# Kernel tuning notes

Hardware: AMD Instinct MI355X
Metric: run time of the kernel (lower is better)

The kernel has to match this reference:

```python
import jax, jax.numpy as jnp
import numpy as np

EMBED = 768
HEADS = 12
HEAD_DIM = EMBED // HEADS
DEPTH = 4
PATCH = 16
GRID = 32  # 512 / 16
MLP_DIM = 4 * EMBED
LN_EPS = 1e-5


def layer_norm(x, w, b):
    m = jnp.mean(x, axis=-1, keepdims=True)
    v = jnp.mean(jnp.square(x - m), axis=-1, keepdims=True)
    return (x - m) * jax.lax.rsqrt(v + LN_EPS) * w + b


def sam_attention(x, qkv_w, qkv_b, proj_w, proj_b, rel_pos_h, rel_pos_w):
    B, H, W, C = x.shape
    N = H * W
    scale = HEAD_DIM ** -0.5
    qkv = x.reshape(B, N, C) @ qkv_w + qkv_b  # (B, N, 3C)
    qkv = qkv.reshape(B, N, 3, HEADS, HEAD_DIM).transpose(2, 0, 3, 1, 4)
    qkv = qkv.reshape(3, B * HEADS, N, HEAD_DIM)
    q, k, v = qkv[0], qkv[1], qkv[2]
    attn = jnp.einsum('bqc,bkc->bqk', q * scale, k)  # (B*nh, N, N)
    # decomposed relative position (q_size == k_size, table already max_rel_dist)
    idx_h = jnp.arange(H)[:, None] - jnp.arange(H)[None, :] + (H - 1)
    idx_w = jnp.arange(W)[:, None] - jnp.arange(W)[None, :] + (W - 1)
    Rh = rel_pos_h[idx_h]  # (H, H, hd)
    Rw = rel_pos_w[idx_w]  # (W, W, hd)
    r_q = q.reshape(B * HEADS, H, W, HEAD_DIM)
    rel_h = jnp.einsum('bhwc,hkc->bhwk', r_q, Rh)
    rel_w = jnp.einsum('bhwc,wkc->bhwk', r_q, Rw)
    attn = (attn.reshape(B * HEADS, H, W, H, W)
            + rel_h[:, :, :, :, None]
            + rel_w[:, :, :, None, :]).reshape(B * HEADS, N, N)
    attn = jax.nn.softmax(attn, axis=-1)
    out = (attn @ v).reshape(B, HEADS, H, W, HEAD_DIM)
    out = out.transpose(0, 2, 3, 1, 4).reshape(B, H, W, C)
    return out @ proj_w + proj_b


def setup_inputs() -> dict:
    key = jax.random.key(0)
    ks = jax.random.split(key, 20)
    s = lambda k, shape, sc=0.02: jax.random.normal(k, shape, jnp.float32) * sc
    inp = {
        'x': jax.random.normal(ks[0], (4, 3, 512, 512), jnp.float32),
        'conv_w': s(ks[1], (EMBED, 3, PATCH, PATCH)),
        'conv_b': jnp.zeros((EMBED,), jnp.float32),
        'pos_embed': s(ks[2], (1, GRID, GRID, EMBED)),
        'ln1_w': jnp.ones((DEPTH, EMBED), jnp.float32),
        'ln1_b': jnp.zeros((DEPTH, EMBED), jnp.float32),
        'qkv_w': s(ks[3], (DEPTH, EMBED, 3 * EMBED)),
        'qkv_b': jnp.zeros((DEPTH, 3 * EMBED), jnp.float32),
        'proj_w': s(ks[4], (DEPTH, EMBED, EMBED)),
        'proj_b': jnp.zeros((DEPTH, EMBED), jnp.float32),
        'rel_pos_h': s(ks[5], (DEPTH, 2 * GRID - 1, HEAD_DIM)),
        'rel_pos_w': s(ks[6], (DEPTH, 2 * GRID - 1, HEAD_DIM)),
        'ln2_w': jnp.ones((DEPTH, EMBED), jnp.float32),
        'ln2_b': jnp.zeros((DEPTH, EMBED), jnp.float32),
        'fc1_w': s(ks[7], (DEPTH, EMBED, MLP_DIM)),
        'fc1_b': jnp.zeros((DEPTH, MLP_DIM), jnp.float32),
        'fc2_w': s(ks[8], (DEPTH, MLP_DIM, EMBED)),
        'fc2_b': jnp.zeros((DEPTH, EMBED), jnp.float32),
    }
    return inp


def reference(x, conv_w, conv_b, pos_embed, ln1_w, ln1_b, qkv_w, qkv_b,
              proj_w, proj_b, rel_pos_h, rel_pos_w, ln2_w, ln2_b,
              fc1_w, fc1_b, fc2_w, fc2_b):
    # patch embed: conv stride=patch, then NCHW -> NHWC
    h = jax.lax.conv_general_dilated(
        x, conv_w, window_strides=(PATCH, PATCH), padding='VALID',
        dimension_numbers=('NCHW', 'OIHW', 'NCHW'))
    h = h.transpose(0, 2, 3, 1) + conv_b  # (B, 32, 32, 768)
    h = h + pos_embed
    for i in range(DEPTH):
        a = sam_attention(layer_norm(h, ln1_w[i], ln1_b[i]),
                          qkv_w[i], qkv_b[i], proj_w[i], proj_b[i],
                          rel_pos_h[i], rel_pos_w[i])
        h = h + a
        m = layer_norm(h, ln2_w[i], ln2_b[i])
        m = jax.nn.gelu(m @ fc1_w[i] + fc1_b[i], approximate=False) @ fc2_w[i] + fc2_b[i]
        h = h + m
    return h
```

## Files before the change

kernel.cpp:

```cpp
#include <hip/hip_runtime.h>
#include <hip/hip_bf16.h>
#include <math.h>
#include <stdint.h>

#define EMBED 768
#define NTOK  1024
#define BATCH 4
#define NHEAD 12
#define HD    64
#define MLPD  3072
#define M_ROWS 4096

typedef __attribute__((ext_vector_type(8))) short short8;
typedef __attribute__((ext_vector_type(4))) float floatx4;

__device__ __forceinline__ float b2f(__hip_bfloat16 v) { return __bfloat162float(v); }

__device__ __forceinline__ void gld_lds16(const void* g, void* l) {
    __builtin_amdgcn_global_load_lds(
        (const __attribute__((address_space(1))) uint32_t*)g,
        (__attribute__((address_space(3))) uint32_t*)l, 16, 0, 0);
}

__device__ __forceinline__ int swz(int row, int c) { return row*64 + (((c) ^ (row & 7)) << 3); }

__device__ __forceinline__ void xcd_remap(int gx, int gy, int& bx, int& by) {
    int id  = blockIdx.x + gx*blockIdx.y;
    int nwg = gx*gy;
    int q = nwg >> 3, r = nwg & 7;
    int xcd = id & 7, idx = id >> 3;
    int nid = (xcd < r ? xcd*(q+1) : r*(q+1) + (xcd-r)*q) + idx;
    bx = nid % gx;
    by = nid / gx;
}

__global__ __launch_bounds__(256)
void im2col(const float* __restrict__ x, __hip_bfloat16* __restrict__ A)
{
    int p  = blockIdx.x;
    int b  = p >> 10;
    int n  = p & 1023;
    int gh = n >> 5, gw = n & 31;
    int tid = threadIdx.x;
    for (int i = tid; i < 768; i += 256) {
        int ci = i >> 8, r = i & 255, kh = r >> 4, kw = r & 15;
        A[(size_t)p*768 + i] = __float2bfloat16(
            x[(((size_t)b*3 + ci)*512 + (gh*16 + kh))*512 + gw*16 + kw]);
    }
}

__global__ __launch_bounds__(256)
void cvt_bf16(const float* __restrict__ in, __hip_bfloat16* __restrict__ out, int n)
{
    int i = blockIdx.x*256 + threadIdx.x;
    if (i < n) out[i] = __float2bfloat16(in[i]);
}

__global__ __launch_bounds__(256)
void layernorm_bf16(const float* __restrict__ in,
                    const float* __restrict__ w,
                    const float* __restrict__ b,
                    __hip_bfloat16* __restrict__ out)
{
    int row = blockIdx.x;
    const float* xr = in + (size_t)row*768;
    int tid = threadIdx.x;
    float v0 = xr[tid], v1 = xr[tid+256], v2 = xr[tid+512];
    float s = v0+v1+v2, ss = v0*v0+v1*v1+v2*v2;
    __shared__ float rs[256], rss[256];
    rs[tid] = s; rss[tid] = ss; __syncthreads();
    for (int o = 128; o > 0; o >>= 1) {
        if (tid < o) { rs[tid] += rs[tid+o]; rss[tid] += rss[tid+o]; }
        __syncthreads();
    }
    float mean = rs[0] * (1.f/768.f);
    float var  = rss[0] * (1.f/768.f) - mean*mean;
    float inv  = rsqrtf(var + 1e-5f);
    out[(size_t)row*768 + tid]     = __float2bfloat16((v0-mean)*inv*w[tid]     + b[tid]);
    out[(size_t)row*768 + tid+256] = __float2bfloat16((v1-mean)*inv*w[tid+256] + b[tid+256]);
    out[(size_t)row*768 + tid+512] = __float2bfloat16((v2-mean)*inv*w[tid+512] + b[tid+512]);
}

__global__ __launch_bounds__(256)
void resum_ln(float* __restrict__ h,
              const float* __restrict__ p0, const float* __restrict__ p1,
              const float* __restrict__ bias,
              const float* __restrict__ w, const float* __restrict__ b,
              __hip_bfloat16* __restrict__ out)
{
    int row = blockIdx.x;
    int tid = threadIdx.x;
    size_t base = (size_t)row*768;
    float v[3];
    float s = 0.f, ss = 0.f;
    #pragma unroll
    for (int e = 0; e < 3; ++e) {
        int i = tid + e*256;
        float val = h[base+i] + p0[base+i] + p1[base+i] + bias[i];
        h[base+i] = val;
        v[e] = val; s += val; ss += val*val;
    }
    __shared__ float rs[256], rss[256];
    rs[tid] = s; rss[tid] = ss; __syncthreads();
    for (int o = 128; o > 0; o >>= 1) {
        if (tid < o) { rs[tid] += rs[tid+o]; rss[tid] += rss[tid+o]; }
        __syncthreads();
    }
    float mean = rs[0] * (1.f/768.f);
    float var  = rss[0] * (1.f/768.f) - mean*mean;
    float inv  = rsqrtf(var + 1e-5f);
    #pragma unroll
    for (int e = 0; e < 3; ++e) {
        int i = tid + e*256;
        out[base+i] = __float2bfloat16((v[e]-mean)*inv*w[i] + b[i]);
    }
}

__global__ __launch_bounds__(256)
void resum_out(const float* __restrict__ h,
               const float* __restrict__ p0, const float* __restrict__ p1,
               const float* __restrict__ bias,
               float* __restrict__ out)
{
    int i = blockIdx.x*256 + threadIdx.x;
    out[i] = h[i] + p0[i] + p1[i] + bias[i % 768];
}

__global__ __launch_bounds__(256)
void prep_weights(const float* __restrict__ qkv_w,  const float* __restrict__ proj_w,
                  const float* __restrict__ fc1_w,  const float* __restrict__ fc2_w,
                  __hip_bfloat16* __restrict__ qkv_wt, __hip_bfloat16* __restrict__ proj_wt,
                  __hip_bfloat16* __restrict__ fc1_wt, __hip_bfloat16* __restrict__ fc2_wt)
{
    int id = blockIdx.x;
    const float* src; __hip_bfloat16* dst; int K, N, bx, by;
    if (id < 1728)      {            src = qkv_w;  dst = qkv_wt;  K = 768;  N = 2304; bx = id % 72; by = id / 72; }
    else if (id < 2304) { id -= 1728; src = proj_w; dst = proj_wt; K = 768;  N = 768;  bx = id % 24; by = id / 24; }
    else if (id < 4608) { id -= 2304; src = fc1_w;  dst = fc1_wt;  K = 768;  N = 3072; bx = id % 96; by = id / 96; }
    else                { id -= 4608; src = fc2_w;  dst = fc2_wt;  K = 3072; N = 768;  bx = id % 24; by = id / 24; }

    __shared__ float t[32][33];
    int n0 = bx*32, k0 = by*32;
    int tx = threadIdx.x & 31, ty = threadIdx.x >> 5;
    #pragma unroll
    for (int r = 0; r < 4; ++r) {
        int row = ty + r*8;
        t[row][tx] = src[(size_t)(k0+row)*N + n0 + tx];
    }
    __syncthreads();
    #pragma unroll
    for (int r = 0; r < 4; ++r) {
        int row = ty + r*8;
        dst[(size_t)(n0+row)*K + k0 + tx] = __float2bfloat16(t[tx][row]);
    }
}

__global__ __launch_bounds__(256)
void gemm64(const __hip_bfloat16* __restrict__ A,
            const __hip_bfloat16* __restrict__ Bt,
            const float* __restrict__ bias,
            const float* __restrict__ res,
            const float* __restrict__ posadd,
            float* __restrict__ Cf,
            int M, int N, int K)
{
    __shared__ __align__(16) char smem[24576];

    const int tid  = threadIdx.x;
    const int lane = tid & 63;
    const int wid  = tid >> 6;
    const int wr   = wid >> 1;
    const int wc   = wid & 1;
    const int lr   = lane & 15;
    const int quad = lane >> 4;

    int bx, by;
    xcd_remap(gridDim.x, gridDim.y, bx, by);
    const int bm = by * 64;
    const int bn = bx * 128;

    const int srow  = tid >> 2;
    const int skoff = ((tid & 3) ^ ((tid >> 3) & 3)) * 8;
    const int csw   = (quad ^ ((lr >> 1) & 3)) * 8;

    floatx4 acc[2][4];
    #pragma unroll
    for (int i = 0; i < 2; ++i)
        #pragma unroll
        for (int j = 0; j < 4; ++j)
            acc[i][j] = (floatx4){0.f,0.f,0.f,0.f};

    auto stage = [&](int bq, int k0) {
        char* base = smem + bq*12288 + (wid * 1024);
        gld_lds16(A + (size_t)(bm + srow)*K + k0 + skoff, base);
        #pragma unroll
        for (int c = 0; c < 2; ++c)
            gld_lds16(Bt + (size_t)(bn + c*64 + srow)*K + k0 + skoff,
                      base + 4096 + c*4096);
    };

    const int nt = K >> 5;
    stage(0, 0);
    stage(1, 32);
    int cur = 0;
    for (int t = 0; t < nt; ++t) {
        if (t + 1 < nt) asm volatile("s_waitcnt vmcnt(3)" ::: "memory");
        else            asm volatile("s_waitcnt vmcnt(0)" ::: "memory");
        __builtin_amdgcn_s_barrier();

        const __hip_bfloat16* As = (const __hip_bfloat16*)(smem + cur*12288);
        const __hip_bfloat16* Bs = As + 2048;

        short8 a[2], b[4];
        #pragma unroll
        for (int i = 0; i < 2; ++i)
            a[i] = *(const short8*)((const void*)(As + (wr*32 + i*16 + lr)*32 + csw));
        #pragma unroll
        for (int j = 0; j < 4; ++j)
            b[j] = *(const short8*)((const void*)(Bs + (wc*64 + j*16 + lr)*32 + csw));
        asm volatile("s_waitcnt lgkmcnt(0)" ::: "memory");
        __builtin_amdgcn_sched_barrier(0);
        __builtin_amdgcn_s_barrier();

        if (t + 2 < nt) stage(cur, (t+2)*32);

        #pragma unroll
        for (int i = 0; i < 2; ++i)
            #pragma unroll
            for (int j = 0; j < 4; ++j)
                acc[i][j] = __builtin_amdgcn_mfma_f32_16x16x32_bf16(a[i], b[j], acc[i][j], 0, 0, 0);
        cur ^= 1;
    }

    #pragma unroll
    for (int j = 0; j < 4; ++j) {
        int col = bn + wc*64 + j*16 + lr;
        float bs = bias[col];
        #pragma unroll
        for (int i = 0; i < 2; ++i) {
            #pragma unroll
            for (int r = 0; r < 4; ++r) {
                int row = bm + wr*32 + i*16 + quad*4 + r;
                float val = acc[i][j][r] + bs;
                if (res)    val += res[(size_t)row*N + col];
                if (posadd) val += posadd[(size_t)(row & 1023)*N + col];
                Cf[(size_t)row*N + col] = val;
            }
        }
    }
}

__global__ __launch_bounds__(256)
void gemm128(const __hip_bfloat16* __restrict__ A,
             const __hip_bfloat16* __restrict__ Bt,
             const float* __restrict__ bias,
             float* __restrict__ Cf,
             __hip_bfloat16* __restrict__ Cb,
             __hip_bfloat16* __restrict__ qp,
             __hip_bfloat16* __restrict__ kp,
             __hip_bfloat16* __restrict__ vp,
             int M, int N, int K, int S, int dogelu, int emode)
{
    __shared__ __align__(16) char smem[32768];

    const int tid  = threadIdx.x;
    const int lane = tid & 63;
    const int wid  = tid >> 6;
    const int wr   = wid >> 1;
    const int wc   = wid & 1;
    const int lr   = lane & 15;
    const int quad = lane >> 4;

    int bx, by;
    xcd_remap(gridDim.x, gridDim.y, bx, by);
    const int bm = by * 128;
    const int bn = bx * 128;
    const int z  = blockIdx.z;
    const int Kseg = K / S;
    const int kbeg = z * Kseg;

    const int srow  = tid >> 2;
    const int skoff = ((tid & 3) ^ ((tid >> 3) & 3)) * 8;
    const int csw   = (quad ^ ((lr >> 1) & 3)) * 8;

    floatx4 acc[4][4];
    #pragma unroll
    for (int i = 0; i < 4; ++i)
        #pragma unroll
        for (int j = 0; j < 4; ++j)
            acc[i][j] = (floatx4){0.f,0.f,0.f,0.f};

    auto stage = [&](int bq, int k0) {
        char* base = smem + bq*16384 + (wid * 1024);
        #pragma unroll
        for (int c = 0; c < 2; ++c)
            gld_lds16(A + (size_t)(bm + c*64 + srow)*K + k0 + skoff,
                      base + c*4096);
        #pragma unroll
        for (int c = 0; c < 2; ++c)
            gld_lds16(Bt + (size_t)(bn + c*64 + srow)*K + k0 + skoff,
                      base + 8192 + c*4096);
    };

    const int nt = Kseg >> 5;
    stage(0, kbeg);
    stage(1, kbeg + 32);
    int cur = 0;
    for (int t = 0; t < nt; ++t) {
        if (t + 1 < nt) asm volatile("s_waitcnt vmcnt(4)" ::: "memory");
        else            asm volatile("s_waitcnt vmcnt(0)" ::: "memory");
        __builtin_amdgcn_s_barrier();

        const __hip_bfloat16* As = (const __hip_bfloat16*)(smem + cur*16384);
        const __hip_bfloat16* Bs = As + 4096;

        short8 a[4], b[4];
        #pragma unroll
        for (int i = 0; i < 4; ++i)
            a[i] = *(const short8*)((const void*)(As + (wr*64 + i*16 + lr)*32 + csw));
        #pragma unroll
        for (int j = 0; j < 4; ++j)
            b[j] = *(const short8*)((const void*)(Bs + (wc*64 + j*16 + lr)*32 + csw));
        asm volatile("s_waitcnt lgkmcnt(0)" ::: "memory");
        __builtin_amdgcn_sched_barrier(0);
        __builtin_amdgcn_s_barrier();

        if (t + 2 < nt) stage(cur, kbeg + (t+2)*32);

        #pragma unroll
        for (int i = 0; i < 4; ++i)
            #pragma unroll
            for (int j = 0; j < 4; ++j)
                acc[i][j] = __builtin_amdgcn_mfma_f32_16x16x32_bf16(a[i], b[j], acc[i][j], 0, 0, 0);
        cur ^= 1;
    }

    if (emode == 3) {
        #pragma unroll
        for (int j = 0; j < 4; ++j) {
            int col = bn + wc*64 + j*16 + lr;
            #pragma unroll
            for (int i = 0; i < 4; ++i) {
                #pragma unroll
                for (int r = 0; r < 4; ++r) {
                    int row = bm + wr*64 + i*16 + quad*4 + r;
                    Cf[(size_t)z*M*N + (size_t)row*N + col] = acc[i][j][r];
                }
            }
        }
        return;
    }

    __hip_bfloat16* epi = (__hip_bfloat16*)(smem + wid*4864);

    if (emode == 1) {
        #pragma unroll
        for (int p = 0; p < 2; ++p) {
            #pragma unroll
            for (int j = 0; j < 4; ++j) {
                float bs = bias[bn + wc*64 + j*16 + lr];
                #pragma unroll
                for (int ii = 0; ii < 2; ++ii) {
                    int i = p*2 + ii;
                    #pragma unroll
                    for (int r = 0; r < 4; ++r) {
                        float val = acc[i][j][r] + bs;
                        if (dogelu) val = 0.5f*val*(1.f + erff(val*0.70710678118f));
                        epi[(ii*16 + quad*4 + r)*72 + j*16 + lr] = __float2bfloat16(val);
                    }
                }
            }
            #pragma unroll
            for (int p2 = 0; p2 < 4; ++p2) {
                int row = p2*8 + (lane >> 3), chunk = lane & 7;
                short8 v = *(const short8*)((const void*)(epi + row*72 + chunk*8));
                *(short8*)((void*)(Cb + (size_t)(bm + wr*64 + p*32 + row)*N
                                      + bn + wc*64 + chunk*8)) = v;
            }
        }
        return;
    }

    const int head64 = (bn + wc*64) >> 6;
    const int which  = head64 / 12;
    const int head   = head64 % 12;
    const int b_     = (bm + wr*64) >> 10;
    const int bh     = b_*NHEAD + head;
    const int n0     = (bm + wr*64) & 1023;

    if (which < 2) {
        __hip_bfloat16* dst = (which == 0 ? qp : kp) + ((size_t)bh*NTOK + n0)*HD;
        #pragma unroll
        for (int p = 0; p < 2; ++p) {
            #pragma unroll
            for (int j = 0; j < 4; ++j) {
                float bs = bias[bn + wc*64 + j*16 + lr];
                #pragma unroll
                for (int ii = 0; ii < 2; ++ii) {
                    int i = p*2 + ii;
                    #pragma unroll
                    for (int r = 0; r < 4; ++r)
                        epi[(ii*16 + quad*4 + r)*72 + j*16 + lr] =
                            __float2bfloat16(acc[i][j][r] + bs);
                }
            }
            #pragma unroll
            for (int p2 = 0; p2 < 4; ++p2) {
                int row = p2*8 + (lane >> 3), chunk = lane & 7;
                short8 v = *(const short8*)((const void*)(epi + row*72 + chunk*8));
                *(short8*)((void*)(dst + (size_t)(p*32 + row)*HD + chunk*8)) = v;
            }
        }
    } else {
        __hip_bfloat16* dstv = vp + (size_t)bh*HD*NTOK + n0;
        #pragma unroll
        for (int p = 0; p < 2; ++p) {
            #pragma unroll
            for (int j = 0; j < 4; ++j) {
                float bs = bias[bn + wc*64 + j*16 + lr];
                #pragma unroll
                for (int ii = 0; ii < 2; ++ii) {
                    int i = p*2 + ii;
                    #pragma unroll
                    for (int r = 0; r < 4; ++r)
                        epi[(j*16 + lr)*36 + ii*16 + quad*4 + r] =
                            __float2bfloat16(acc[i][j][r] + bs);
                }
            }
            #pragma unroll
            for (int p2 = 0; p2 < 4; ++p2) {
                int d = p2*16 + (lane >> 2), chunk = lane & 3;
                short8 v = *(const short8*)((const void*)(epi + d*36 + chunk*8));
                *(short8*)((void*)(dstv + (size_t)d*NTOK + p*32 + chunk*8)) = v;
            }
        }
    }
}

__global__ __launch_bounds__(256)
void attention_mfma(const __hip_bfloat16* __restrict__ qp,
                    const __hip_bfloat16* __restrict__ kp,
                    const __hip_bfloat16* __restrict__ vp,
                    const float* __restrict__ rph,
                    const float* __restrict__ rpw,
                    __hip_bfloat16* __restrict__ out)
{
    const int blk  = blockIdx.x;
    const int bh   = blk >> 4;
    const int qt   = blk & 15;
    const int b    = bh / NHEAD;
    const int head = bh % NHEAD;
    const int tid  = threadIdx.x;
    const int lane = tid & 63;
    const int w    = tid >> 6;
    const int lr   = lane & 15;
    const int quad = lane >> 4;

    __shared__ __align__(16) __hip_bfloat16 Qs[64*64];
    __shared__ __align__(16) __hip_bfloat16 Ks[64*64];
    __shared__ __align__(16) __hip_bfloat16 Vs[64*64];
    __shared__ __align__(16) __hip_bfloat16 Ps[4*16*64];
    __shared__ float relhS[64*32];
    __shared__ float relwS[64*32];

    const __hip_bfloat16* qb = qp + ((size_t)bh*NTOK + qt*64)*HD;
    const __hip_bfloat16* kb = kp + (size_t)bh*NTOK*HD;
    const __hip_bfloat16* vb = vp + (size_t)bh*HD*NTOK;

    const int sr = tid >> 2;
    const int sc = (tid & 3) * 2;

    short8 kreg0, kreg1, vreg0, vreg1;
    {
        const __hip_bfloat16* kk = kb + (size_t)sr*HD + sc*8;
        kreg0 = *(const short8*)((const void*)kk);
        kreg1 = *(const short8*)((const void*)(kk + 8));
        const __hip_bfloat16* vv = vb + (size_t)sr*NTOK + sc*8;
        vreg0 = *(const short8*)((const void*)vv);
        vreg1 = *(const short8*)((const void*)(vv + 8));
    }

    {
        const __hip_bfloat16* qq = qb + (size_t)sr*HD + sc*8;
        short8 q0 = *(const short8*)((const void*)qq);
        short8 q1 = *(const short8*)((const void*)(qq + 8));
        *(short8*)((void*)(Qs + swz(sr, sc)))   = q0;
        *(short8*)((void*)(Qs + swz(sr, sc+1))) = q1;
    }

    for (int i = tid; i < 504; i += 256) {
        int r = i >> 3, c = i & 7;
        const float* ph = rph + (size_t)r*HD + c*8;
        const float* pw = rpw + (size_t)r*HD + c*8;
        union { short8 v; __hip_bfloat16 e[8]; } uh, uw;
        #pragma unroll
        for (int e = 0; e < 8; ++e) { uh.e[e] = __float2bfloat16(ph[e]); uw.e[e] = __float2bfloat16(pw[e]); }
        *(short8*)((void*)(Ks + swz(r, c))) = uh.v;
        *(short8*)((void*)(Vs + swz(r, c))) = uw.v;
    }
    if (tid < 16) {
        short8 z = (short8){0,0,0,0,0,0,0,0};
        int c = tid & 7;
        if (tid < 8) *(short8*)((void*)(Ks + swz(63, c))) = z;
        else         *(short8*)((void*)(Vs + swz(63, c))) = z;
    }
    __syncthreads();

    short8 qa0 = *(const short8*)((const void*)(Qs + swz(w*16 + lr, quad)));
    short8 qa1 = *(const short8*)((const void*)(Qs + swz(w*16 + lr, 4 + quad)));

    const int qrow = w*16 + quad*4;
    const int qh_  = qt*2 + (w >> 1);
    const int qw_  = (w & 1)*16 + quad*4;

    #pragma unroll
    for (int j = 0; j < 4; ++j) {
        int t = j*16 + lr;
        short8 th0 = *(const short8*)((const void*)(Ks + swz(j*16 + lr, quad)));
        short8 th1 = *(const short8*)((const void*)(Ks + swz(j*16 + lr, 4 + quad)));
        floatx4 ha = (floatx4){0.f,0.f,0.f,0.f};
        ha = __builtin_amdgcn_mfma_f32_16x16x32_bf16(qa0, th0, ha, 0, 0, 0);
        ha = __builtin_amdgcn_mfma_f32_16x16x32_bf16(qa1, th1, ha, 0, 0, 0);
        short8 tw0 = *(const short8*)((const void*)(Vs + swz(j*16 + lr, quad)));
        short8 tw1 = *(const short8*)((const void*)(Vs + swz(j*16 + lr, 4 + quad)));
        floatx4 wa = (floatx4){0.f,0.f,0.f,0.f};
        wa = __builtin_amdgcn_mfma_f32_16x16x32_bf16(qa0, tw0, wa, 0, 0, 0);
        wa = __builtin_amdgcn_mfma_f32_16x16x32_bf16(qa1, tw1, wa, 0, 0, 0);
        int kh = qh_ + 31 - t;
        #pragma unroll
        for (int rr = 0; rr < 4; ++rr) {
            if (kh >= 0 && kh < 32) relhS[(qrow + rr)*32 + kh] = ha[rr];
            int kw = qw_ + rr + 31 - t;
            if (kw >= 0 && kw < 32) relwS[(qrow + rr)*32 + kw] = wa[rr];
        }
    }

    float rw[4][2];
    #pragma unroll
    for (int rr = 0; rr < 4; ++rr)
        #pragma unroll
        for (int jp = 0; jp < 2; ++jp)
            rw[rr][jp] = relwS[(qrow + rr)*32 + jp*16 + lr];

    floatx4 o[4];
    #pragma unroll
    for (int ds = 0; ds < 4; ++ds) o[ds] = (floatx4){0.f,0.f,0.f,0.f};
    float lsum[4] = {0.f, 0.f, 0.f, 0.f};

    const float scale = 0.125f;

    for (int kt = 0; kt < 16; ++kt) {
        __syncthreads();
        *(short8*)((void*)(Ks + swz(sr, sc)))   = kreg0;
        *(short8*)((void*)(Ks + swz(sr, sc+1))) = kreg1;
        *(short8*)((void*)(Vs + swz(sr, sc)))   = vreg0;
        *(short8*)((void*)(Vs + swz(sr, sc+1))) = vreg1;
        __syncthreads();

        if (kt < 15) {
            const __hip_bfloat16* kk = kb + (size_t)(kt+1)*64*HD + (size_t)sr*HD + sc*8;
            kreg0 = *(const short8*)((const void*)kk);
            kreg1 = *(const short8*)((const void*)(kk + 8));
            const __hip_bfloat16* vv = vb + (size_t)sr*NTOK + (kt+1)*64 + sc*8;
            vreg0 = *(const short8*)((const void*)vv);
            vreg1 = *(const short8*)((const void*)(vv + 8));
        }

        float2 rh2[4];
        #pragma unroll
        for (int rr = 0; rr < 4; ++rr)
            rh2[rr] = *(const float2*)((const void*)(relhS + (qrow + rr)*32 + kt*2));

        floatx4 sv[4];
        #pragma unroll
        for (int j = 0; j < 4; ++j) {
            short8 kb0 = *(const short8*)((const void*)(Ks + swz(j*16 + lr, quad)));
            short8 kb1 = *(const short8*)((const void*)(Ks + swz(j*16 + lr, 4 + quad)));
            floatx4 z = (floatx4){0.f,0.f,0.f,0.f};
            z = __builtin_amdgcn_mfma_f32_16x16x32_bf16(qa0, kb0, z, 0, 0, 0);
            z = __builtin_amdgcn_mfma_f32_16x16x32_bf16(qa1, kb1, z, 0, 0, 0);
            sv[j] = z;
        }

        #pragma unroll
        for (int j = 0; j < 4; ++j) {
            int colc = j*2 + (lr >> 3);
            #pragma unroll
            for (int rr = 0; rr < 4; ++rr) {
                float s = sv[j][rr]*scale + ((j < 2) ? rh2[rr].x : rh2[rr].y) + rw[rr][j & 1];
                s = fminf(fmaxf(s, -60.f), 60.f);
                float pp = __expf(s);
                lsum[rr] += pp;
                int prow = quad*4 + rr;
                Ps[w*1024 + prow*64 + ((colc ^ (prow & 7)) << 3) + (lr & 7)] = __float2bfloat16(pp);
            }
        }

        short8 pa0 = *(const short8*)((const void*)(Ps + w*1024 + swz(lr, quad)));
        short8 pa1 = *(const short8*)((const void*)(Ps + w*1024 + swz(lr, 4 + quad)));
        #pragma unroll
        for (int ds = 0; ds < 4; ++ds) {
            short8 v0 = *(const short8*)((const void*)(Vs + swz(ds*16 + lr, quad)));
            short8 v1 = *(const short8*)((const void*)(Vs + swz(ds*16 + lr, 4 + quad)));
            o[ds] = __builtin_amdgcn_mfma_f32_16x16x32_bf16(pa0, v0, o[ds], 0, 0, 0);
            o[ds] = __builtin_amdgcn_mfma_f32_16x16x32_bf16(pa1, v1, o[ds], 0, 0, 0);
        }
    }

    #pragma unroll
    for (int off = 1; off < 16; off <<= 1)
        #pragma unroll
        for (int rr = 0; rr < 4; ++rr)
            lsum[rr] += __shfl_xor(lsum[rr], off, 16);

    #pragma unroll
    for (int rr = 0; rr < 4; ++rr) {
        float inv = 1.f / lsum[rr];
        int n = qt*64 + w*16 + quad*4 + rr;
        size_t base = ((size_t)b*NTOK + n)*EMBED + head*HD;
        #pragma unroll
        for (int ds = 0; ds < 4; ++ds)
            out[base + ds*16 + lr] = __float2bfloat16(o[ds][rr] * inv);
    }
}

extern "C" void kernel_launch(void* const* d_in, const int* in_sizes, int n_in,
                              void* d_out, int out_size, void* d_ws, size_t ws_size,
                              hipStream_t stream)
{
    const float* x      = (const float*)d_in[0];
    const float* conv_w = (const float*)d_in[1];
    const float* conv_b = (const float*)d_in[2];
    const float* pos    = (const float*)d_in[3];
    const float* ln1_w  = (const float*)d_in[4];
    const float* ln1_b  = (const float*)d_in[5];
    const float* qkv_w  = (const float*)d_in[6];
    const float* qkv_b  = (const float*)d_in[7];
    const float* proj_w = (const float*)d_in[8];
    const float* proj_b = (const float*)d_in[9];
    const float* rph    = (const float*)d_in[10];
    const float* rpw    = (const float*)d_in[11];
    const float* ln2_w  = (const float*)d_in[12];
    const float* ln2_b  = (const float*)d_in[13];
    const float* fc1_w  = (const float*)d_in[14];
    const float* fc1_b  = (const float*)d_in[15];
    const float* fc2_w  = (const float*)d_in[16];
    const float* fc2_b  = (const float*)d_in[17];

    char* p = (char*)d_ws;
    float*           h       = (float*)p;           p += (size_t)M_ROWS*EMBED*4;
    __hip_bfloat16*  q_perm  = (__hip_bfloat16*)p;
    float*           p0      = (float*)p;           p += (size_t)48*NTOK*HD*2;
    __hip_bfloat16*  k_perm  = (__hip_bfloat16*)p;  p += (size_t)48*NTOK*HD*2;
    __hip_bfloat16*  vt_perm = (__hip_bfloat16*)p;  p += (size_t)48*NTOK*HD*2;
    __hip_bfloat16*  attn_o  = (__hip_bfloat16*)p;  p += (size_t)M_ROWS*EMBED*2;
    __hip_bfloat16*  x_ln    = (__hip_bfloat16*)p;  p += (size_t)M_ROWS*EMBED*2;
    __hip_bfloat16*  mlp     = (__hip_bfloat16*)p;  p += (size_t)M_ROWS*MLPD*2;
    __hip_bfloat16*  qkv_wt  = (__hip_bfloat16*)p;  p += (size_t)2304*768*2;
    __hip_bfloat16*  proj_wt = (__hip_bfloat16*)p;  p += (size_t)768*768*2;
    __hip_bfloat16*  fc1_wt  = (__hip_bfloat16*)p;  p += (size_t)MLPD*768*2;
    __hip_bfloat16*  fc2_wt  = (__hip_bfloat16*)p;  p += (size_t)768*MLPD*2;

    __hip_bfloat16*  A_im    = mlp;
    __hip_bfloat16*  conv_wt = qkv_wt;

    im2col<<<M_ROWS, 256, 0, stream>>>(x, A_im);
    cvt_bf16<<<(768*768 + 255)/256, 256, 0, stream>>>(conv_w, conv_wt, 768*768);
    gemm64<<<dim3(768/128, M_ROWS/64, 1), 256, 0, stream>>>(
        A_im, conv_wt, conv_b, nullptr, pos, h, M_ROWS, 768, 768);

    layernorm_bf16<<<M_ROWS, 256, 0, stream>>>(h, ln1_w, ln1_b, x_ln);

    for (int L = 0; L < 4; ++L) {
        prep_weights<<<6912, 256, 0, stream>>>(
            qkv_w + (size_t)L*768*2304, proj_w + (size_t)L*768*768,
            fc1_w + (size_t)L*768*MLPD, fc2_w + (size_t)L*MLPD*768,
            qkv_wt, proj_wt, fc1_wt, fc2_wt);

        gemm128<<<dim3(2304/128, M_ROWS/128, 1), 256, 0, stream>>>(
            x_ln, qkv_wt, qkv_b + (size_t)L*3*EMBED,
            nullptr, nullptr, q_perm, k_perm, vt_perm,
            M_ROWS, 2304, 768, 1, 0, 2);

        attention_mfma<<<48*16, 256, 0, stream>>>(
            q_perm, k_perm, vt_perm,
            rph + (size_t)L*63*64, rpw + (size_t)L*63*64, attn_o);

        gemm64<<<dim3(768/128, M_ROWS/64, 1), 256, 0, stream>>>(
            attn_o, proj_wt, proj_b + (size_t)L*EMBED, h, nullptr,
            h, M_ROWS, 768, 768);

        layernorm_bf16<<<M_ROWS, 256, 0, stream>>>(h, ln2_w + L*EMBED, ln2_b + L*EMBED, x_ln);

        gemm128<<<dim3(MLPD/128, M_ROWS/128, 1), 256, 0, stream>>>(
            x_ln, fc1_wt, fc1_b + (size_t)L*MLPD,
            nullptr, mlp, nullptr, nullptr, nullptr,
            M_ROWS, MLPD, 768, 1, 1, 1);

        gemm128<<<dim3(768/128, M_ROWS/128, 2), 256, 0, stream>>>(
            mlp, fc2_wt, nullptr,
            p0, nullptr, nullptr, nullptr, nullptr,
            M_ROWS, 768, MLPD, 2, 0, 3);

        float* p1 = p0 + (size_t)M_ROWS*768;
        if (L < 3) {
            resum_ln<<<M_ROWS, 256, 0, stream>>>(
                h, p0, p1, fc2_b + (size_t)L*EMBED,
                ln1_w + (size_t)(L+1)*EMBED, ln1_b + (size_t)(L+1)*EMBED, x_ln);
        } else {
            resum_out<<<M_ROWS*EMBED/256, 256, 0, stream>>>(
                h, p0, p1, fc2_b + (size_t)L*EMBED, (float*)d_out);
        }
    }
}
```

Measured before the change: 898.0 us.

## Triple-buffer LDS and double-buffer register fragments in GEMM main loops

Both GEMM kernels go from a two-stage LDS ring to a three-stage ring, and the loop is unrolled by two with ping-pong register fragments. LDS reads for the next K-step are issued before the MFMAs of the current step, so LDS latency overlaps with matrix math, and global prefetch runs one tile further ahead. The cost is more shared memory per block (36KB and 48KB), which may lower occupancy, plus extra registers for the second fragment set. The loop assumes an even number of K tiles per segment.

Result: slower. 920.8 us (+2.5%).

```diff
diff --git a/kernel.cpp b/kernel.cpp
--- a/kernel.cpp
+++ b/kernel.cpp
@@ -164,7 +164,7 @@
             float* __restrict__ Cf,
             int M, int N, int K)
 {
-    __shared__ __align__(16) char smem[24576];
+    __shared__ __align__(16) char smem[36864];
 
     const int tid  = threadIdx.x;
     const int lane = tid & 63;
@@ -198,38 +198,59 @@
             gld_lds16(Bt + (size_t)(bn + c*64 + srow)*K + k0 + skoff,
                       base + 4096 + c*4096);
     };
-
-    const int nt = K >> 5;
-    stage(0, 0);
-    stage(1, 32);
-    int cur = 0;
-    for (int t = 0; t < nt; ++t) {
-        if (t + 1 < nt) asm volatile("s_waitcnt vmcnt(3)" ::: "memory");
-        else            asm volatile("s_waitcnt vmcnt(0)" ::: "memory");
-        __builtin_amdgcn_s_barrier();
-
-        const __hip_bfloat16* As = (const __hip_bfloat16*)(smem + cur*12288);
+    auto ldread = [&](short8* a, short8* b, int bq) {
+        const __hip_bfloat16* As = (const __hip_bfloat16*)(smem + bq*12288);
         const __hip_bfloat16* Bs = As + 2048;
-
-        short8 a[2], b[4];
         #pragma unroll
         for (int i = 0; i < 2; ++i)
             a[i] = *(const short8*)((const void*)(As + (wr*32 + i*16 + lr)*32 + csw));
         #pragma unroll
         for (int j = 0; j < 4; ++j)
             b[j] = *(const short8*)((const void*)(Bs + (wc*64 + j*16 + lr)*32 + csw));
+    };
+    auto mfma8 = [&](short8* a, short8* b) {
+        #pragma unroll
+        for (int i = 0; i < 2; ++i)
+            #pragma unroll
+            for (int j = 0; j < 4; ++j)
+                acc[i][j] = __builtin_amdgcn_mfma_f32_16x16x32_bf16(a[i], b[j], acc[i][j], 0, 0, 0);
+    };
+
+    const int nt = K >> 5;
+    stage(0, 0); stage(1, 32); stage(2, 64);
+    asm volatile("s_waitcnt vmcnt(6)" ::: "memory");
+    __builtin_amdgcn_s_barrier();
+    __builtin_amdgcn_sched_barrier(0);
+
+    short8 aA[2], bA[4], aB[2], bB[4];
+    ldread(aA, bA, 0);
+
+    int rb = 1;
+    int sb = 0;
+    for (int t = 0; t < nt; t += 2) {
         asm volatile("s_waitcnt lgkmcnt(0)" ::: "memory");
         __builtin_amdgcn_sched_barrier(0);
+        if (t + 3 <= nt) asm volatile("s_waitcnt vmcnt(3)" ::: "memory");
+        else             asm volatile("s_waitcnt vmcnt(0)" ::: "memory");
         __builtin_amdgcn_s_barrier();
-
-        if (t + 2 < nt) stage(cur, (t+2)*32);
-
-        #pragma unroll
-        for (int i = 0; i < 2; ++i)
-            #pragma unroll
-            for (int j = 0; j < 4; ++j)
-                acc[i][j] = __builtin_amdgcn_mfma_f32_16x16x32_bf16(a[i], b[j], acc[i][j], 0, 0, 0);
-        cur ^= 1;
+        __builtin_amdgcn_sched_barrier(0);
+        ldread(aB, bB, rb);
+        if (t + 3 < nt) stage(sb, (t+3)*32);
+        mfma8(aA, bA);
+        rb = (rb == 2) ? 0 : rb + 1;
+        sb = (sb == 2) ? 0 : sb + 1;
+
+        asm volatile("s_waitcnt lgkmcnt(0)" ::: "memory");
+        __builtin_amdgcn_sched_barrier(0);
+        if (t + 4 <= nt) asm volatile("s_waitcnt vmcnt(3)" ::: "memory");
+        else             asm volatile("s_waitcnt vmcnt(0)" ::: "memory");
+        __builtin_amdgcn_s_barrier();
+        __builtin_amdgcn_sched_barrier(0);
+        if (t + 2 < nt) ldread(aA, bA, rb);
+        if (t + 4 < nt) stage(sb, (t+4)*32);
+        mfma8(aB, bB);
+        rb = (rb == 2) ? 0 : rb + 1;
+        sb = (sb == 2) ? 0 : sb + 1;
     }
 
     #pragma unroll
@@ -261,7 +282,7 @@
              __hip_bfloat16* __restrict__ vp,
              int M, int N, int K, int S, int dogelu, int emode)
 {
-    __shared__ __align__(16) char smem[32768];
+    __shared__ __align__(16) char smem[49152];
 
     const int tid  = threadIdx.x;
     const int lane = tid & 63;
@@ -301,38 +322,59 @@
             gld_lds16(Bt + (size_t)(bn + c*64 + srow)*K + k0 + skoff,
                       base + 8192 + c*4096);
     };
-
-    const int nt = Kseg >> 5;
-    stage(0, kbeg);
-    stage(1, kbeg + 32);
-    int cur = 0;
-    for (int t = 0; t < nt; ++t) {
-        if (t + 1 < nt) asm volatile("s_waitcnt vmcnt(4)" ::: "memory");
-        else            asm volatile("s_waitcnt vmcnt(0)" ::: "memory");
-        __builtin_amdgcn_s_barrier();
-
-        const __hip_bfloat16* As = (const __hip_bfloat16*)(smem + cur*16384);
+    auto ldread = [&](short8* a, short8* b, int bq) {
+        const __hip_bfloat16* As = (const __hip_bfloat16*)(smem + bq*16384);
         const __hip_bfloat16* Bs = As + 4096;
-
-        short8 a[4], b[4];
         #pragma unroll
         for (int i = 0; i < 4; ++i)
             a[i] = *(const short8*)((const void*)(As + (wr*64 + i*16 + lr)*32 + csw));
         #pragma unroll
         for (int j = 0; j < 4; ++j)
             b[j] = *(const short8*)((const void*)(Bs + (wc*64 + j*16 + lr)*32 + csw));
+    };
+    auto mfma16 = [&](short8* a, short8* b) {
+        #pragma unroll
+        for (int i = 0; i < 4; ++i)
+            #pragma unroll
+            for (int j = 0; j < 4; ++j)
+                acc[i][j] = __builtin_amdgcn_mfma_f32_16x16x32_bf16(a[i], b[j], acc[i][j], 0, 0, 0);
+    };
+
+    const int nt = Kseg >> 5;
+    stage(0, kbeg); stage(1, kbeg + 32); stage(2, kbeg + 64);
+    asm volatile("s_waitcnt vmcnt(8)" ::: "memory");
+    __builtin_amdgcn_s_barrier();
+    __builtin_amdgcn_sched_barrier(0);
+
+    short8 aA[4], bA[4], aB[4], bB[4];
+    ldread(aA, bA, 0);
+
+    int rb = 1;
+    int sb = 0;
+    for (int t = 0; t < nt; t += 2) {
         asm volatile("s_waitcnt lgkmcnt(0)" ::: "memory");
         __builtin_amdgcn_sched_barrier(0);
+        if (t + 3 <= nt) asm volatile("s_waitcnt vmcnt(4)" ::: "memory");
+        else             asm volatile("s_waitcnt vmcnt(0)" ::: "memory");
         __builtin_amdgcn_s_barrier();
-
-        if (t + 2 < nt) stage(cur, kbeg + (t+2)*32);
-
-        #pragma unroll
-        for (int i = 0; i < 4; ++i)
-            #pragma unroll
-            for (int j = 0; j < 4; ++j)
-                acc[i][j] = __builtin_amdgcn_mfma_f32_16x16x32_bf16(a[i], b[j], acc[i][j], 0, 0, 0);
-        cur ^= 1;
+        __builtin_amdgcn_sched_barrier(0);
+        ldread(aB, bB, rb);
+        if (t + 3 < nt) stage(sb, kbeg + (t+3)*32);
+        mfma16(aA, bA);
+        rb = (rb == 2) ? 0 : rb + 1;
+        sb = (sb == 2) ? 0 : sb + 1;
+
+        asm volatile("s_waitcnt lgkmcnt(0)" ::: "memory");
+        __builtin_amdgcn_sched_barrier(0);
+        if (t + 4 <= nt) asm volatile("s_waitcnt vmcnt(4)" ::: "memory");
+        else             asm volatile("s_waitcnt vmcnt(0)" ::: "memory");
+        __builtin_amdgcn_s_barrier();
+        __builtin_amdgcn_sched_barrier(0);
+        if (t + 2 < nt) ldread(aA, bA, rb);
+        if (t + 4 < nt) stage(sb, kbeg + (t+4)*32);
+        mfma16(aB, bB);
+        rb = (rb == 2) ? 0 : rb + 1;
+        sb = (sb == 2) ? 0 : sb + 1;
     }
 
     if (emode == 3) {
```
